# Optimization experiments

Hardware: AMD Instinct MI355X
Metric: run time of the kernel (lower is better)

## Reference

```python
import jax, jax.numpy as jnp
import numpy as np

NEG_SLOPE = 0.2  # PyG GATConv default negative_slope


def gat_layer(x, src, dst, W, b, att_src, att_dst, heads, concat):
    """PyG-style GATConv (eval mode, self-loops already in src/dst).
    x: [N, F_in], W: [F_in, heads*hd], att_*: [heads, hd], b: [out_dim].
    """
    N = x.shape[0]
    hd = W.shape[1] // heads
    h = (x @ W).reshape(N, heads, hd)                      # [N, H, D]
    a_s = jnp.einsum('nhd,hd->nh', h, att_src)             # [N, H]
    a_d = jnp.einsum('nhd,hd->nh', h, att_dst)             # [N, H]
    e = jax.nn.leaky_relu(a_s[src] + a_d[dst], NEG_SLOPE)  # [E, H]
    # segment softmax over edges sharing a destination node
    m = jax.ops.segment_max(e, dst, num_segments=N)        # [N, H]
    m = jnp.where(jnp.isfinite(m), m, 0.0)
    ex = jnp.exp(e - m[dst])
    den = jax.ops.segment_sum(ex, dst, num_segments=N)     # [N, H]
    alpha = ex / (den[dst] + 1e-16)                        # [E, H]
    out = jax.ops.segment_sum(h[src] * alpha[:, :, None], dst, num_segments=N)  # [N,H,D]
    out = out.reshape(N, heads * hd) if concat else out.mean(axis=1)
    return out + b


def setup_inputs() -> dict:
    key = jax.random.key(0)
    ks = jax.random.split(key, 16)
    N, E, F_IN, HID, H, C = 100000, 1600000, 256, 128, 8, 6
    HD = HID // H
    s = 0.1
    return {
        'x': jax.random.normal(ks[0], (N, F_IN), jnp.float32),
        'edge_index': jax.random.randint(ks[1], (2, E), 0, N, jnp.int64),
        'W1': jax.random.normal(ks[2], (F_IN, HID), jnp.float32) * s,
        'b1': jnp.zeros((HID,), jnp.float32),
        'att_src1': jax.random.normal(ks[3], (H, HD), jnp.float32) * s,
        'att_dst1': jax.random.normal(ks[4], (H, HD), jnp.float32) * s,
        'W2': jax.random.normal(ks[5], (HID, HID), jnp.float32) * s,
        'b2': jnp.zeros((HID,), jnp.float32),
        'att_src2': jax.random.normal(ks[6], (H, HD), jnp.float32) * s,
        'att_dst2': jax.random.normal(ks[7], (H, HD), jnp.float32) * s,
        'W3': jax.random.normal(ks[8], (HID, C), jnp.float32) * s,
        'b3': jnp.zeros((C,), jnp.float32),
        'att_src3': jax.random.normal(ks[9], (1, C), jnp.float32) * s,
        'att_dst3': jax.random.normal(ks[10], (1, C), jnp.float32) * s,
    }


def reference(x, edge_index, W1, b1, att_src1, att_dst1, W2, b2, att_src2, att_dst2,
              W3, b3, att_src3, att_dst3):
    N = x.shape[0]
    loops = jnp.arange(N, dtype=edge_index.dtype)
    src = jnp.concatenate([edge_index[0], loops])  # add self-loops (PyG default)
    dst = jnp.concatenate([edge_index[1], loops])
    h = jax.nn.elu(gat_layer(x, src, dst, W1, b1, att_src1, att_dst1, 8, True))
    h = jax.nn.elu(gat_layer(h, src, dst, W2, b2, att_src2, att_dst2, 8, True))
    return gat_layer(h, src, dst, W3, b3, att_src3, att_dst3, 1, False)
```

## Files before the change

### kernel.cpp

```cpp
#include <hip/hip_runtime.h>
#include <hip/hip_bf16.h>
#include <cstdint>

typedef unsigned short u16;
typedef __attribute__((ext_vector_type(8))) short bf16x8;
typedef __attribute__((ext_vector_type(4))) float f32x4;

#define CAP 48

__device__ __forceinline__ float b2f(u16 u){
  union { unsigned int i; float f; } v; v.i = ((unsigned int)u) << 16; return v.f;
}
__device__ __forceinline__ u16 f2b(float f){
  union { float f; unsigned int i; } v; v.f = f;
  unsigned int x = v.i;
  x += 0x7fff + ((x >> 16) & 1);
  return (u16)(x >> 16);
}
__device__ __forceinline__ float lrelu(float x){ return x > 0.f ? x : 0.2f * x; }

__global__ void k_flags(const u16* __restrict__ xr, const int* __restrict__ ei,
                        int* __restrict__ flags){
  __shared__ float smax[256];
  int t = threadIdx.x;
  float v = fabsf(b2f(xr[t * 2]));
  if (!isfinite(v)) v = 1e30f;
  smax[t] = v;
  __syncthreads();
  for (int off = 128; off > 0; off >>= 1){
    if (t < off) smax[t] = fmaxf(smax[t], smax[t + off]);
    __syncthreads();
  }
  if (t == 0){
    flags[0] = (smax[0] > 1e4f) ? 1 : 0;
    int allz = 1;
    for (int i = 1; i < 32; i += 2) if (ei[i] != 0) allz = 0;
    flags[1] = allz;
    flags[2] = 0;
    flags[3] = 0;
  }
}

#define PW_W1 0
#define PW_B1 32768
#define PW_AS1 32896
#define PW_AD1 33024
#define PW_W2 33152
#define PW_B2 49536
#define PW_AS2 49664
#define PW_AD2 49792
#define PW_W3 49920
#define PW_B3 50688
#define PW_AS3 50694
#define PW_AD3 50700
#define PW_TOTAL 50706

__global__ void k_cvt_params(const void* p0, const void* p1, const void* p2, const void* p3,
                             const void* p4, const void* p5, const void* p6, const void* p7,
                             const void* p8, const void* p9, const void* p10, const void* p11,
                             u16* __restrict__ pw, const int* __restrict__ flags){
  int i = blockIdx.x * blockDim.x + threadIdx.x;
  if (i >= PW_TOTAL) return;
  const int sizes[12] = {32768,128,128,128,16384,128,128,128,768,6,6,6};
  const void* ptrs[12] = {p0,p1,p2,p3,p4,p5,p6,p7,p8,p9,p10,p11};
  int off = 0, seg = 0, loc = 0;
  for (int s = 0; s < 12; s++){
    if (i < off + sizes[s]){ seg = s; loc = i - off; break; }
    off += sizes[s];
  }
  float v = flags[0] ? ((const float*)ptrs[seg])[loc] : b2f(((const u16*)ptrs[seg])[loc]);
  pw[i] = f2b(v);
}

__global__ void k_transpose(const u16* __restrict__ src, u16* __restrict__ dst, int R, int C){
  int i = blockIdx.x * blockDim.x + threadIdx.x;
  if (i >= R * C) return;
  int r = i / C, c = i - r * C;
  dst[(size_t)c * R + r] = src[i];
}

__device__ __forceinline__ int eread(const int* __restrict__ ei, int idx, int is64){
  return ei[is64 ? (idx << 1) : idx];
}

__global__ __launch_bounds__(256) void k_scatter_gemm1(const int* __restrict__ ei, int E,
                                                       int* __restrict__ cnt, int* __restrict__ ebuf,
                                                       const int* __restrict__ flags, int SB,
                                                       const void* __restrict__ Xv,
                                                       const u16* __restrict__ WT,
                                                       u16* __restrict__ Ho, int N){
  if ((int)blockIdx.x < SB){
    int is64 = flags[1];
    for (int i = blockIdx.x * blockDim.x + threadIdx.x; i < E; i += SB * blockDim.x){
      int s = eread(ei, i, is64);
      int d = eread(ei, E + i, is64);
      int pos = atomicAdd(&cnt[d], 1);
      if (pos < CAP) ebuf[d * CAP + pos] = s;
    }
    return;
  }
  constexpr int K = 256;
  int bid = (int)blockIdx.x - SB;
  int gwave = (bid * 256 + (int)threadIdx.x) >> 6;
  int lane = threadIdx.x & 63;
  int n0 = gwave * 32;
  if (n0 >= N) return;
  int quad = lane >> 4, l15 = lane & 15;
  int r0 = n0 + l15;        if (r0 >= N) r0 = N - 1;
  int r1 = n0 + 16 + l15;   if (r1 >= N) r1 = N - 1;
  const u16* wbase = WT + (size_t)l15 * K + quad * 8;
  f32x4 acc[2][8] = {};
  if (flags[0]){
    const float* x0p = (const float*)Xv + (size_t)r0 * K + quad * 8;
    const float* x1p = (const float*)Xv + (size_t)r1 * K + quad * 8;
    for (int k0 = 0; k0 < K; k0 += 32){
      float4 v00 = *(const float4*)(x0p + k0);
      float4 v01 = *(const float4*)(x0p + k0 + 4);
      float4 v10 = *(const float4*)(x1p + k0);
      float4 v11 = *(const float4*)(x1p + k0 + 4);
      bf16x8 a0, a1;
      a0[0]=(short)f2b(v00.x); a0[1]=(short)f2b(v00.y); a0[2]=(short)f2b(v00.z); a0[3]=(short)f2b(v00.w);
      a0[4]=(short)f2b(v01.x); a0[5]=(short)f2b(v01.y); a0[6]=(short)f2b(v01.z); a0[7]=(short)f2b(v01.w);
      a1[0]=(short)f2b(v10.x); a1[1]=(short)f2b(v10.y); a1[2]=(short)f2b(v10.z); a1[3]=(short)f2b(v10.w);
      a1[4]=(short)f2b(v11.x); a1[5]=(short)f2b(v11.y); a1[6]=(short)f2b(v11.z); a1[7]=(short)f2b(v11.w);
      #pragma unroll
      for (int c = 0; c < 8; c++){
        bf16x8 b = *(const bf16x8*)(wbase + (size_t)c * 16 * K + k0);
        acc[0][c] = __builtin_amdgcn_mfma_f32_16x16x32_bf16(a0, b, acc[0][c], 0, 0, 0);
        acc[1][c] = __builtin_amdgcn_mfma_f32_16x16x32_bf16(a1, b, acc[1][c], 0, 0, 0);
      }
    }
  } else {
    const u16* x0p = (const u16*)Xv + (size_t)r0 * K + quad * 8;
    const u16* x1p = (const u16*)Xv + (size_t)r1 * K + quad * 8;
    for (int k0 = 0; k0 < K; k0 += 32){
      bf16x8 a0 = *(const bf16x8*)(x0p + k0);
      bf16x8 a1 = *(const bf16x8*)(x1p + k0);
      #pragma unroll
      for (int c = 0; c < 8; c++){
        bf16x8 b = *(const bf16x8*)(wbase + (size_t)c * 16 * K + k0);
        acc[0][c] = __builtin_amdgcn_mfma_f32_16x16x32_bf16(a0, b, acc[0][c], 0, 0, 0);
        acc[1][c] = __builtin_amdgcn_mfma_f32_16x16x32_bf16(a1, b, acc[1][c], 0, 0, 0);
      }
    }
  }
  #pragma unroll
  for (int t = 0; t < 2; t++){
    #pragma unroll
    for (int c = 0; c < 8; c++){
      #pragma unroll
      for (int r = 0; r < 4; r++){
        int row = n0 + t * 16 + quad * 4 + r;
        if (row < N) Ho[(size_t)row * 128 + c * 16 + l15] = f2b(acc[t][c][r]);
      }
    }
  }
}

template<int K>
__global__ __launch_bounds__(256) void k_gemm_mfma(const void* __restrict__ Xv,
                                                   const u16* __restrict__ WT,
                                                   u16* __restrict__ Ho, int N,
                                                   const int* __restrict__ flags){
  int gwave = (blockIdx.x * blockDim.x + threadIdx.x) >> 6;
  int lane = threadIdx.x & 63;
  int n0 = gwave * 32;
  if (n0 >= N) return;
  int quad = lane >> 4, l15 = lane & 15;
  int r0 = n0 + l15;        if (r0 >= N) r0 = N - 1;
  int r1 = n0 + 16 + l15;   if (r1 >= N) r1 = N - 1;
  const u16* wbase = WT + (size_t)l15 * K + quad * 8;
  f32x4 acc[2][8] = {};
  const u16* x0p = (const u16*)Xv + (size_t)r0 * K + quad * 8;
  const u16* x1p = (const u16*)Xv + (size_t)r1 * K + quad * 8;
  for (int k0 = 0; k0 < K; k0 += 32){
    bf16x8 a0 = *(const bf16x8*)(x0p + k0);
    bf16x8 a1 = *(const bf16x8*)(x1p + k0);
    #pragma unroll
    for (int c = 0; c < 8; c++){
      bf16x8 b = *(const bf16x8*)(wbase + (size_t)c * 16 * K + k0);
      acc[0][c] = __builtin_amdgcn_mfma_f32_16x16x32_bf16(a0, b, acc[0][c], 0, 0, 0);
      acc[1][c] = __builtin_amdgcn_mfma_f32_16x16x32_bf16(a1, b, acc[1][c], 0, 0, 0);
    }
  }
  #pragma unroll
  for (int t = 0; t < 2; t++){
    #pragma unroll
    for (int c = 0; c < 8; c++){
      #pragma unroll
      for (int r = 0; r < 4; r++){
        int row = n0 + t * 16 + quad * 4 + r;
        if (row < N) Ho[(size_t)row * 128 + c * 16 + l15] = f2b(acc[t][c][r]);
      }
    }
  }
}

__global__ __launch_bounds__(256) void k_gemm3(const u16* __restrict__ X, const u16* __restrict__ W,
                                               u16* __restrict__ Ho, int N){
  __shared__ float sW[128 * 6];
  for (int i = threadIdx.x; i < 128 * 6; i += blockDim.x) sW[i] = b2f(W[i]);
  __syncthreads();
  int n = blockIdx.x * blockDim.x + threadIdx.x;
  if (n >= N) return;
  const u16* xr = X + (size_t)n * 128;
  float acc[6] = {0, 0, 0, 0, 0, 0};
  #pragma unroll 8
  for (int k = 0; k < 128; k += 2){
    unsigned int xp = *(const unsigned int*)(xr + k);
    float x0 = b2f((u16)(xp & 0xffff));
    float x1 = b2f((u16)(xp >> 16));
    const float* w0 = sW + k * 6;
    #pragma unroll
    for (int j = 0; j < 6; j++) acc[j] += x0 * w0[j] + x1 * w0[6 + j];
  }
  u16* out = Ho + (size_t)n * 6;
  #pragma unroll
  for (int j = 0; j < 6; j++) out[j] = f2b(acc[j]);
}

template<int H, int D>
__global__ __launch_bounds__(256) void k_att(const u16* __restrict__ Hbuf,
                                             const u16* __restrict__ AS, const u16* __restrict__ AD,
                                             float* __restrict__ as_o, float* __restrict__ ad_o, int N){
  int t = blockIdx.x * blockDim.x + threadIdx.x;
  if (t >= N * H) return;
  int n = t / H, h = t - n * H;
  const u16* hp = Hbuf + (size_t)n * (H * D) + h * D;
  float s1 = 0, s2 = 0;
  #pragma unroll
  for (int d = 0; d < D; d++){
    float v = b2f(hp[d]);
    s1 += v * b2f(AS[h * D + d]);
    s2 += v * b2f(AD[h * D + d]);
  }
  as_o[t] = s1; ad_o[t] = s2;
}

template<int H, int D, int EPI>
__global__ __launch_bounds__(256) void k_agg(const u16* __restrict__ Hbuf, const float* __restrict__ as,
                                             const float* __restrict__ ad,
                                             const int* __restrict__ cnt, const int* __restrict__ ebuf,
                                             const u16* __restrict__ bias, void* __restrict__ outv,
                                             const int* __restrict__ flags, int N){
  constexpr int DP = D / 2;
  constexpr int LPN = H * DP;
  constexpr int NPW = 64 / LPN;
  int wave = (blockIdx.x * blockDim.x + threadIdx.x) >> 6;
  int lane = threadIdx.x & 63;
  int sub = lane / LPN;
  int rem = lane - sub * LPN;
  int n = wave * NPW + sub;
  if (sub >= NPW || n >= N) return;
  int head = rem / DP, dp = rem - head * DP;
  int nh = n * H + head;
  float adi = ad[nh];
  size_t hoff = (size_t)head * D + 2 * dp;
  float w = __expf(lrelu(as[nh] + adi));
  unsigned int hp = *(const unsigned int*)(Hbuf + (size_t)n * (H * D) + hoff);
  float den = w;
  float a0 = w * b2f((u16)(hp & 0xffff));
  float a1 = w * b2f((u16)(hp >> 16));
  int deg = cnt[n]; if (deg > CAP) deg = CAP;
  const int* row = ebuf + n * CAP;
  int j = 0;
  for (; j + 4 <= deg; j += 4){
    int s0 = row[j], s1 = row[j + 1], s2 = row[j + 2], s3 = row[j + 3];
    float v0 = as[s0 * H + head];
    float v1 = as[s1 * H + head];
    float v2 = as[s2 * H + head];
    float v3 = as[s3 * H + head];
    unsigned int q0 = *(const unsigned int*)(Hbuf + (size_t)s0 * (H * D) + hoff);
    unsigned int q1 = *(const unsigned int*)(Hbuf + (size_t)s1 * (H * D) + hoff);
    unsigned int q2 = *(const unsigned int*)(Hbuf + (size_t)s2 * (H * D) + hoff);
    unsigned int q3 = *(const unsigned int*)(Hbuf + (size_t)s3 * (H * D) + hoff);
    float w0 = __expf(lrelu(v0 + adi));
    float w1 = __expf(lrelu(v1 + adi));
    float w2 = __expf(lrelu(v2 + adi));
    float w3 = __expf(lrelu(v3 + adi));
    den += (w0 + w1) + (w2 + w3);
    a0 += w0 * b2f((u16)(q0 & 0xffff)) + w1 * b2f((u16)(q1 & 0xffff))
        + w2 * b2f((u16)(q2 & 0xffff)) + w3 * b2f((u16)(q3 & 0xffff));
    a1 += w0 * b2f((u16)(q0 >> 16)) + w1 * b2f((u16)(q1 >> 16))
        + w2 * b2f((u16)(q2 >> 16)) + w3 * b2f((u16)(q3 >> 16));
  }
  for (; j < deg; j++){
    int s = row[j];
    float w2 = __expf(lrelu(as[s * H + head] + adi));
    unsigned int hq = *(const unsigned int*)(Hbuf + (size_t)s * (H * D) + hoff);
    den += w2;
    a0 += w2 * b2f((u16)(hq & 0xffff));
    a1 += w2 * b2f((u16)(hq >> 16));
  }
  float inv = 1.f / (den + 1e-16f);
  a0 *= inv; a1 *= inv;
  int jidx = head * D + 2 * dp;
  a0 += b2f(bias[jidx]);
  a1 += b2f(bias[jidx + 1]);
  if (EPI == 0){
    a0 = a0 > 0.f ? a0 : expm1f(a0);
    a1 = a1 > 0.f ? a1 : expm1f(a1);
    unsigned int packed = (unsigned int)f2b(a0) | ((unsigned int)f2b(a1) << 16);
    *(unsigned int*)((u16*)outv + (size_t)n * (H * D) + jidx) = packed;
  } else {
    if (flags[0]){
      float2* o = (float2*)((float*)outv + (size_t)n * (H * D) + jidx);
      *o = make_float2(a0, a1);
    } else {
      unsigned int packed = (unsigned int)f2b(a0) | ((unsigned int)f2b(a1) << 16);
      *(unsigned int*)((u16*)outv + (size_t)n * (H * D) + jidx) = packed;
    }
  }
}

extern "C" void kernel_launch(void* const* d_in, const int* in_sizes, int n_in,
                              void* d_out, int out_size, void* d_ws, size_t ws_size,
                              hipStream_t stream){
  const void* x   = d_in[0];
  const int*  ei  = (const int*)d_in[1];

  const int N = in_sizes[0] / 256;
  const int E = in_sizes[1] / 2;

  char* p = (char*)d_ws;
  auto alloc = [&](size_t bytes){ void* q = (void*)p; p += (bytes + 255) & ~(size_t)255; return q; };
  int*   flags  = (int*)alloc(256);
  int*   cnt    = (int*)alloc((size_t)N * 4);
  int*   ebuf   = (int*)alloc((size_t)N * CAP * 4);
  u16*   hbuf   = (u16*)alloc((size_t)N * 128 * 2);
  float* asb    = (float*)alloc((size_t)N * 8 * 4);
  float* adb    = (float*)alloc((size_t)N * 8 * 4);
  u16*   x2     = (u16*)alloc((size_t)N * 128 * 2);
  u16*   x3     = (u16*)alloc((size_t)N * 128 * 2);
  u16*   pw     = (u16*)alloc((size_t)PW_TOTAL * 2);
  u16*   wt1    = (u16*)alloc((size_t)128 * 256 * 2);
  u16*   wt2    = (u16*)alloc((size_t)128 * 128 * 2);

  const int tb = 256;

  k_flags<<<1, 256, 0, stream>>>((const u16*)x, ei, flags);
  k_cvt_params<<<(PW_TOTAL + tb - 1) / tb, tb, 0, stream>>>(
      d_in[2], d_in[3], d_in[4], d_in[5], d_in[6], d_in[7],
      d_in[8], d_in[9], d_in[10], d_in[11], d_in[12], d_in[13], pw, flags);
  k_transpose<<<(32768 + tb - 1) / tb, tb, 0, stream>>>(pw + PW_W1, wt1, 256, 128);
  k_transpose<<<(16384 + tb - 1) / tb, tb, 0, stream>>>(pw + PW_W2, wt2, 128, 128);
  hipMemsetAsync(cnt, 0, (size_t)N * 4, stream);

  int gemm_blocks = (N + 127) / 128;
  const int SB = 1024;

  k_scatter_gemm1<<<SB + gemm_blocks, tb, 0, stream>>>(ei, E, cnt, ebuf, flags, SB,
                                                       x, wt1, hbuf, N);
  k_att<8, 16><<<(N * 8 + tb - 1) / tb, tb, 0, stream>>>(hbuf, pw + PW_AS1, pw + PW_AD1, asb, adb, N);
  k_agg<8, 16, 0><<<((size_t)N * 64 + tb - 1) / tb, tb, 0, stream>>>(hbuf, asb, adb, cnt, ebuf, pw + PW_B1, x2, flags, N);

  k_gemm_mfma<128><<<gemm_blocks, tb, 0, stream>>>(x2, wt2, hbuf, N, flags + 2);
  k_att<8, 16><<<(N * 8 + tb - 1) / tb, tb, 0, stream>>>(hbuf, pw + PW_AS2, pw + PW_AD2, asb, adb, N);
  k_agg<8, 16, 0><<<((size_t)N * 64 + tb - 1) / tb, tb, 0, stream>>>(hbuf, asb, adb, cnt, ebuf, pw + PW_B2, x3, flags, N);

  k_gemm3<<<(N + tb - 1) / tb, tb, 0, stream>>>(x3, pw + PW_W3, hbuf, N);
  k_att<1, 6><<<(N + tb - 1) / tb, tb, 0, stream>>>(hbuf, pw + PW_AS3, pw + PW_AD3, asb, adb, N);
  int waves3 = (N + 20) / 21;
  k_agg<1, 6, 1><<<((size_t)waves3 * 64 + tb - 1) / tb, tb, 0, stream>>>(hbuf, asb, adb, cnt, ebuf, pw + PW_B3, d_out, flags, N);
}
```

Measured before the change: 547.6 us.

## Partition edge scatter by destination range per block group; unroll aggregation by eight

The edge scatter now splits its blocks into eight groups. Each group scans all edges but only inserts edges whose destination lies in its eighth of the node range. The aim is locality: atomics and ebuf writes from a group go to a compact address range (likely one XCD's L2), instead of spreading across all nodes. The cost is that the destination index array is read eight times. Separately, the aggregation inner loop is unrolled from four to eight neighbors, putting more independent gathers in flight at the cost of extra registers.

```diff
diff --git a/kernel.cpp b/kernel.cpp
--- a/kernel.cpp
+++ b/kernel.cpp
@@ -85,17 +85,24 @@
 
 __global__ __launch_bounds__(256) void k_scatter_gemm1(const int* __restrict__ ei, int E,
                                                        int* __restrict__ cnt, int* __restrict__ ebuf,
-                                                       const int* __restrict__ flags, int SB,
+                                                       const int* __restrict__ flags, int SB, int octsz,
                                                        const void* __restrict__ Xv,
                                                        const u16* __restrict__ WT,
                                                        u16* __restrict__ Ho, int N){
   if ((int)blockIdx.x < SB){
     int is64 = flags[1];
-    for (int i = blockIdx.x * blockDim.x + threadIdx.x; i < E; i += SB * blockDim.x){
-      int s = eread(ei, i, is64);
+    int SBG = SB >> 3;
+    int g = (int)blockIdx.x / SBG;
+    int lo = g * octsz;
+    int tid = ((int)blockIdx.x - g * SBG) * 256 + (int)threadIdx.x;
+    int stride = SBG * 256;
+    for (int i = tid; i < E; i += stride){
       int d = eread(ei, E + i, is64);
-      int pos = atomicAdd(&cnt[d], 1);
-      if (pos < CAP) ebuf[d * CAP + pos] = s;
+      if ((unsigned)(d - lo) < (unsigned)octsz){
+        int s = eread(ei, i, is64);
+        int pos = atomicAdd(&cnt[d], 1);
+        if (pos < CAP) ebuf[d * CAP + pos] = s;
+      }
     }
     return;
   }
@@ -264,25 +271,34 @@
   int deg = cnt[n]; if (deg > CAP) deg = CAP;
   const int* row = ebuf + n * CAP;
   int j = 0;
-  for (; j + 4 <= deg; j += 4){
-    int s0 = row[j], s1 = row[j + 1], s2 = row[j + 2], s3 = row[j + 3];
-    float v0 = as[s0 * H + head];
-    float v1 = as[s1 * H + head];
-    float v2 = as[s2 * H + head];
-    float v3 = as[s3 * H + head];
+  for (; j + 8 <= deg; j += 8){
+    int s0 = row[j],     s1 = row[j + 1], s2 = row[j + 2], s3 = row[j + 3];
+    int s4 = row[j + 4], s5 = row[j + 5], s6 = row[j + 6], s7 = row[j + 7];
+    float v0 = as[s0 * H + head], v1 = as[s1 * H + head];
+    float v2 = as[s2 * H + head], v3 = as[s3 * H + head];
+    float v4 = as[s4 * H + head], v5 = as[s5 * H + head];
+    float v6 = as[s6 * H + head], v7 = as[s7 * H + head];
     unsigned int q0 = *(const unsigned int*)(Hbuf + (size_t)s0 * (H * D) + hoff);
     unsigned int q1 = *(const unsigned int*)(Hbuf + (size_t)s1 * (H * D) + hoff);
     unsigned int q2 = *(const unsigned int*)(Hbuf + (size_t)s2 * (H * D) + hoff);
     unsigned int q3 = *(const unsigned int*)(Hbuf + (size_t)s3 * (H * D) + hoff);
-    float w0 = __expf(lrelu(v0 + adi));
-    float w1 = __expf(lrelu(v1 + adi));
-    float w2 = __expf(lrelu(v2 + adi));
-    float w3 = __expf(lrelu(v3 + adi));
-    den += (w0 + w1) + (w2 + w3);
+    unsigned int q4 = *(const unsigned int*)(Hbuf + (size_t)s4 * (H * D) + hoff);
+    unsigned int q5 = *(const unsigned int*)(Hbuf + (size_t)s5 * (H * D) + hoff);
+    unsigned int q6 = *(const unsigned int*)(Hbuf + (size_t)s6 * (H * D) + hoff);
+    unsigned int q7 = *(const unsigned int*)(Hbuf + (size_t)s7 * (H * D) + hoff);
+    float w0 = __expf(lrelu(v0 + adi)), w1 = __expf(lrelu(v1 + adi));
+    float w2 = __expf(lrelu(v2 + adi)), w3 = __expf(lrelu(v3 + adi));
+    float w4 = __expf(lrelu(v4 + adi)), w5 = __expf(lrelu(v5 + adi));
+    float w6 = __expf(lrelu(v6 + adi)), w7 = __expf(lrelu(v7 + adi));
+    den += ((w0 + w1) + (w2 + w3)) + ((w4 + w5) + (w6 + w7));
     a0 += w0 * b2f((u16)(q0 & 0xffff)) + w1 * b2f((u16)(q1 & 0xffff))
-        + w2 * b2f((u16)(q2 & 0xffff)) + w3 * b2f((u16)(q3 & 0xffff));
+        + w2 * b2f((u16)(q2 & 0xffff)) + w3 * b2f((u16)(q3 & 0xffff))
+        + w4 * b2f((u16)(q4 & 0xffff)) + w5 * b2f((u16)(q5 & 0xffff))
+        + w6 * b2f((u16)(q6 & 0xffff)) + w7 * b2f((u16)(q7 & 0xffff));
     a1 += w0 * b2f((u16)(q0 >> 16)) + w1 * b2f((u16)(q1 >> 16))
-        + w2 * b2f((u16)(q2 >> 16)) + w3 * b2f((u16)(q3 >> 16));
+        + w2 * b2f((u16)(q2 >> 16)) + w3 * b2f((u16)(q3 >> 16))
+        + w4 * b2f((u16)(q4 >> 16)) + w5 * b2f((u16)(q5 >> 16))
+        + w6 * b2f((u16)(q6 >> 16)) + w7 * b2f((u16)(q7 >> 16));
   }
   for (; j < deg; j++){
     int s = row[j];
@@ -348,8 +364,9 @@
 
   int gemm_blocks = (N + 127) / 128;
   const int SB = 1024;
-
-  k_scatter_gemm1<<<SB + gemm_blocks, tb, 0, stream>>>(ei, E, cnt, ebuf, flags, SB,
+  const int octsz = (N + 7) >> 3;
+
+  k_scatter_gemm1<<<SB + gemm_blocks, tb, 0, stream>>>(ei, E, cnt, ebuf, flags, SB, octsz,
                                                        x, wt1, hbuf, N);
   k_att<8, 16><<<(N * 8 + tb - 1) / tb, tb, 0, stream>>>(hbuf, pw + PW_AS1, pw + PW_AD1, asb, adb, N);
   k_agg<8, 16, 0><<<((size_t)N * 64 + tb - 1) / tb, tb, 0, stream>>>(hbuf, asb, adb, cnt, ebuf, pw + PW_B1, x2, flags, N);
```

After: 612.8 us. 1.12x slower.
